# Kernel optimization log

Hardware: AMD Instinct MI355X
Metric: run time of the kernel (lower is better)

## Reference

```python
import jax, jax.numpy as jnp
import numpy as np

N = 50000      # num_nodes
R = 32         # num_relations
H = 16         # hidden channels
C = 16         # num_classes
E = 1600000    # num_edges (avg degree 32)


def setup_inputs() -> dict:
    key = jax.random.key(0)
    ks = jax.random.split(key, 8)
    edge_index = jax.random.randint(ks[0], (2, E), 0, N)
    edge_type = jnp.sort(jax.random.randint(ks[1], (E,), 0, R))
    # per-relation [start, end) slices into the sorted edge list (is_sorted=True)
    starts = jnp.searchsorted(edge_type, jnp.arange(R))
    ends = jnp.searchsorted(edge_type, jnp.arange(R) + 1)
    tensor_slice = jnp.stack([starts, ends], axis=1)
    s = 0.05
    W1 = jax.random.normal(ks[2], (R, N, H), dtype=jnp.float32) * s   # layer-1 per-relation embedding (x=None)
    root1 = jax.random.normal(ks[3], (N, H), dtype=jnp.float32) * s  # root weight acts as embedding when x=None
    bias1 = jax.random.normal(ks[4], (H,), dtype=jnp.float32) * s
    W2 = jax.random.normal(ks[5], (R, H, C), dtype=jnp.float32) * s
    root2 = jax.random.normal(ks[6], (H, C), dtype=jnp.float32) * s
    bias2 = jax.random.normal(ks[7], (C,), dtype=jnp.float32) * s
    return {"edge_index": edge_index, "edge_type": edge_type, "tensor_slice": tensor_slice,
            "W1": W1, "root1": root1, "bias1": bias1,
            "W2": W2, "root2": root2, "bias2": bias2}


def reference(edge_index, edge_type, tensor_slice, W1, root1, bias1, W2, root2, bias2):
    src, dst = edge_index[0], edge_index[1]
    # ---- layer 1: x=None, so per-relation transform is an embedding lookup W1[r][src]
    msg1 = W1[edge_type, src]                                        # [E, H] relation-indexed gather
    h1 = root1 + jax.ops.segment_sum(msg1, dst, num_segments=N) + bias1
    h1 = jax.nn.relu(h1)
    # ---- layer 2: transform all nodes per relation once, then gather per edge
    t = jnp.einsum('nh,rhc->rnc', h1, W2)                            # [R, N, C]
    msg2 = t[edge_type, src]                                         # [E, C]
    h2 = h1 @ root2 + jax.ops.segment_sum(msg2, dst, num_segments=N) + bias2
    return jax.nn.log_softmax(h2, axis=1)
```

## Files before the change

### kernel.cpp

```cpp
#include <hip/hip_runtime.h>
#include <hip/hip_bf16.h>

static constexpr int H = 16;
static constexpr int C = 16;

typedef __attribute__((ext_vector_type(8))) short bf16x8;
typedef __attribute__((ext_vector_type(4))) float f32x4;

static __device__ inline unsigned short f2bf(float x) {
    __hip_bfloat16 b = __float2bfloat16(x);
    return *reinterpret_cast<unsigned short*>(&b);
}
static __device__ inline float bflo(unsigned u) { return __uint_as_float(u << 16); }
static __device__ inline float bfhi(unsigned u) { return __uint_as_float(u & 0xffff0000u); }
static __device__ inline void pk_atomic_bf16(unsigned short* addr, unsigned pk) {
    asm volatile("global_atomic_pk_add_bf16 %0, %1, off" :: "v"(addr), "v"(pk) : "memory");
}

__global__ void k1_scatter(const int* __restrict__ srcv, const int* __restrict__ dstv,
                           const int* __restrict__ etv, const float* __restrict__ W1,
                           unsigned short* __restrict__ acc1, int E, int N) {
    int t = blockIdx.x * blockDim.x + threadIdx.x;
    int g = t >> 3;
    int cp = t & 7;
    int e0 = g << 2;
    if (e0 >= E) return;
    int n = min(4, E - e0);
    int s[4], d[4], r[4];
#pragma unroll
    for (int i = 0; i < 4; ++i) {
        int e = e0 + ((i < n) ? i : 0);
        s[i] = srcv[e]; d[i] = dstv[e]; r[i] = etv[e];
    }
    float2 v[4];
#pragma unroll
    for (int i = 0; i < 4; ++i)
        v[i] = *(const float2*)(W1 + ((size_t)r[i] * N + (size_t)s[i]) * H + (cp << 1));
#pragma unroll
    for (int i = 0; i < 4; ++i)
        if (i < n) {
            unsigned pk = ((unsigned)f2bf(v[i].y) << 16) | f2bf(v[i].x);
            pk_atomic_bf16(acc1 + ((size_t)d[i] << 4) + (cp << 1), pk);
        }
}

__global__ void k2_fin1(const float* __restrict__ root1, const float* __restrict__ bias1,
                        const unsigned short* __restrict__ acc1, float* __restrict__ h1,
                        unsigned int* __restrict__ h1bf, int total4) {
    int i = blockIdx.x * blockDim.x + threadIdx.x;
    if (i >= total4) return;
    float4 rv = ((const float4*)root1)[i];
    uint2 av = ((const uint2*)acc1)[i];
    float4 bv = ((const float4*)bias1)[i & 3];
    float4 o;
    o.x = fmaxf(rv.x + bflo(av.x) + bv.x, 0.0f);
    o.y = fmaxf(rv.y + bfhi(av.x) + bv.y, 0.0f);
    o.z = fmaxf(rv.z + bflo(av.y) + bv.z, 0.0f);
    o.w = fmaxf(rv.w + bfhi(av.y) + bv.w, 0.0f);
    ((float4*)h1)[i] = o;
    uint2 p;
    p.x = ((unsigned)f2bf(o.y) << 16) | f2bf(o.x);
    p.y = ((unsigned)f2bf(o.w) << 16) | f2bf(o.z);
    ((uint2*)h1bf)[i] = p;
}

__global__ void k0_prep(const int* __restrict__ ts, int* __restrict__ chunk_off, int R) {
    if (blockIdx.x == 0 && threadIdx.x == 0) {
        int acc = 0;
        for (int r = 0; r < R; ++r) {
            chunk_off[r] = acc;
            int cnt = ts[2 * r + 1] - ts[2 * r];
            acc += (cnt + 15) >> 4;
        }
        chunk_off[R] = acc;
    }
}

__global__ void k0_cast(const float* __restrict__ W2, unsigned short* __restrict__ w2t,
                        int total ) {
    int i = blockIdx.x * blockDim.x + threadIdx.x;
    if (i >= total) return;
    int r = i >> 8;
    int kc = i & 255;
    int k = kc >> 4;
    int c = kc & 15;
    w2t[(r << 8) + (c << 4) + k] = f2bf(W2[i]);
}

__global__ void k3_mfma(const int* __restrict__ srcv, const int* __restrict__ dstv,
                        const int* __restrict__ ts, const int* __restrict__ chunk_off,
                        const unsigned short* __restrict__ h1bf,
                        const unsigned short* __restrict__ w2t,
                        unsigned short* __restrict__ acc2, int R) {
    int w = (blockIdx.x * blockDim.x + threadIdx.x) >> 6;
    int l = threadIdx.x & 63;
    int total = chunk_off[R];
    if (w >= total) return;
    int lo = 0, hi = R;
    while (hi - lo > 1) {
        int mid = (lo + hi) >> 1;
        if (chunk_off[mid] <= w) lo = mid; else hi = mid;
    }
    int r = lo;
    int e0 = ts[2 * r] + ((w - chunk_off[r]) << 4);
    int eend = ts[2 * r + 1];
    int n_e = min(16, eend - e0);

    int rowA = l & 15;
    int kg = l >> 4;
    int eA = e0 + min(rowA, n_e - 1);
    int s = srcv[eA];

    bf16x8 a = {0, 0, 0, 0, 0, 0, 0, 0};
    bf16x8 b = {0, 0, 0, 0, 0, 0, 0, 0};
    if (kg < 2) {
        a = *(const bf16x8*)(h1bf + ((size_t)s << 4) + (kg << 3));
        b = *(const bf16x8*)(w2t + ((size_t)r << 8) + (rowA << 4) + (kg << 3));
    }
    f32x4 d = {0.f, 0.f, 0.f, 0.f};
    d = __builtin_amdgcn_mfma_f32_16x16x32_bf16(a, b, d, 0, 0, 0);

    int c = l & 15;
#pragma unroll
    for (int j = 0; j < 4; ++j) {
        float o = __shfl_xor(d[j], 1);
        int row = (kg << 2) + j;
        if (((l & 1) == 0) && row < n_e) {
            int dd = dstv[e0 + row];
            unsigned pk = ((unsigned)f2bf(o) << 16) | f2bf(d[j]);
            pk_atomic_bf16(acc2 + ((size_t)dd << 4) + c, pk);
        }
    }
}

__global__ void k4_fin2(const float* __restrict__ h1, const unsigned short* __restrict__ acc2,
                        const float* __restrict__ root2, const float* __restrict__ bias2,
                        float* __restrict__ out, int N) {
    int n = blockIdx.x * blockDim.x + threadIdx.x;
    if (n >= N) return;
    const float* hr = h1 + (size_t)n * H;
    float h[16];
#pragma unroll
    for (int k = 0; k < 16; ++k) h[k] = hr[k];
    const uint4* ap = (const uint4*)(acc2 + (size_t)n * 16);
    uint4 a0 = ap[0], a1 = ap[1];
    float av[16] = {bflo(a0.x), bfhi(a0.x), bflo(a0.y), bfhi(a0.y),
                    bflo(a0.z), bfhi(a0.z), bflo(a0.w), bfhi(a0.w),
                    bflo(a1.x), bfhi(a1.x), bflo(a1.y), bfhi(a1.y),
                    bflo(a1.z), bfhi(a1.z), bflo(a1.w), bfhi(a1.w)};
    float* o = out + (size_t)n * C;
    float z[16];
#pragma unroll
    for (int c = 0; c < 16; ++c) {
        float acc = av[c] + bias2[c];
#pragma unroll
        for (int k = 0; k < 16; ++k) acc += h[k] * root2[k * C + c];
        z[c] = acc;
    }
    float m = z[0];
#pragma unroll
    for (int c = 1; c < 16; ++c) m = fmaxf(m, z[c]);
    float se = 0.f;
#pragma unroll
    for (int c = 0; c < 16; ++c) se += __expf(z[c] - m);
    float lse = m + __logf(se);
#pragma unroll
    for (int c = 0; c < 16; ++c) o[c] = z[c] - lse;
}

extern "C" void kernel_launch(void* const* d_in, const int* in_sizes, int n_in,
                              void* d_out, int out_size, void* d_ws, size_t ws_size,
                              hipStream_t stream) {
    const int*   edge_index   = (const int*)d_in[0];
    const int*   edge_type    = (const int*)d_in[1];
    const int*   tensor_slice = (const int*)d_in[2];
    const float* W1    = (const float*)d_in[3];
    const float* root1 = (const float*)d_in[4];
    const float* bias1 = (const float*)d_in[5];
    const float* W2    = (const float*)d_in[6];
    const float* root2 = (const float*)d_in[7];
    const float* bias2 = (const float*)d_in[8];
    float* out = (float*)d_out;

    const int E = in_sizes[0] / 2;
    const int N = in_sizes[4] / H;
    const int R = in_sizes[2] / 2;
    const int* srcv = edge_index;
    const int* dstv = edge_index + E;

    char* p = (char*)d_ws;
    unsigned short* acc1 = (unsigned short*)p;   p += (size_t)N * 16 * 2;
    float* h1 = (float*)p;                       p += (size_t)N * 16 * 4;
    unsigned short* h1bf = (unsigned short*)p;   p += (size_t)N * 16 * 2;
    unsigned short* w2t = (unsigned short*)p;    p += (size_t)R * 256 * 2;
    unsigned short* acc2 = (unsigned short*)p;   p += (size_t)N * 16 * 2;
    int* chunk_off = (int*)p;

    hipMemsetAsync(acc1, 0, (size_t)N * 16 * 2, stream);
    hipMemsetAsync(acc2, 0, (size_t)N * 16 * 2, stream);

    const int B = 256;
    k0_prep<<<1, 64, 0, stream>>>(tensor_slice, chunk_off, R);
    k0_cast<<<(R * 256 + B - 1) / B, B, 0, stream>>>(W2, w2t, R * 256);
    long long g1 = ((long long)E + 3) / 4;
    long long t1 = g1 * 8;
    k1_scatter<<<(int)((t1 + B - 1) / B), B, 0, stream>>>(srcv, dstv, edge_type, W1, acc1, E, N);
    int total4 = N * H / 4;
    k2_fin1<<<(total4 + B - 1) / B, B, 0, stream>>>(root1, bias1, acc1, h1,
                                                    (unsigned int*)h1bf, total4);
    long long waves_ub = (long long)((E + 15) / 16) + R;
    long long thr = waves_ub * 64;
    k3_mfma<<<(int)((thr + B - 1) / B), B, 0, stream>>>(srcv, dstv, tensor_slice, chunk_off,
                                                        h1bf, w2t, acc2, R);
    k4_fin2<<<(N + B - 1) / B, B, 0, stream>>>(h1, acc2, root2, bias2, out, N);
}
```

Baseline: 197.1 us.

## Batch four MFMA chunks per wave, precompute chunk map, drop fp32 h1

The layer-2 kernel now handles four 16-edge chunks per wave, using a precomputed chunk-to-(edge start, relation, count) map in place of a per-wave binary search. Destination indices are loaded once per row and shared across the wave with shuffles. Layer-1 scatter threads now each process eight edges instead of four, which raises memory-level parallelism. The fp32 h1 buffer is removed and the final kernel reads bf16 h1, cutting write and read traffic at a small precision cost in the root2 term. An extra small kernel launch is added to build the chunk map.

```diff
diff --git a/kernel.cpp b/kernel.cpp
--- a/kernel.cpp
+++ b/kernel.cpp
@@ -23,21 +23,21 @@
     int t = blockIdx.x * blockDim.x + threadIdx.x;
     int g = t >> 3;
     int cp = t & 7;
-    int e0 = g << 2;
+    int e0 = g << 3;
     if (e0 >= E) return;
-    int n = min(4, E - e0);
-    int s[4], d[4], r[4];
-#pragma unroll
-    for (int i = 0; i < 4; ++i) {
+    int n = min(8, E - e0);
+    int s[8], d[8], r[8];
+#pragma unroll
+    for (int i = 0; i < 8; ++i) {
         int e = e0 + ((i < n) ? i : 0);
         s[i] = srcv[e]; d[i] = dstv[e]; r[i] = etv[e];
     }
-    float2 v[4];
-#pragma unroll
-    for (int i = 0; i < 4; ++i)
+    float2 v[8];
+#pragma unroll
+    for (int i = 0; i < 8; ++i)
         v[i] = *(const float2*)(W1 + ((size_t)r[i] * N + (size_t)s[i]) * H + (cp << 1));
 #pragma unroll
-    for (int i = 0; i < 4; ++i)
+    for (int i = 0; i < 8; ++i)
         if (i < n) {
             unsigned pk = ((unsigned)f2bf(v[i].y) << 16) | f2bf(v[i].x);
             pk_atomic_bf16(acc1 + ((size_t)d[i] << 4) + (cp << 1), pk);
@@ -45,7 +45,7 @@
 }
 
 __global__ void k2_fin1(const float* __restrict__ root1, const float* __restrict__ bias1,
-                        const unsigned short* __restrict__ acc1, float* __restrict__ h1,
+                        const unsigned short* __restrict__ acc1,
                         unsigned int* __restrict__ h1bf, int total4) {
     int i = blockIdx.x * blockDim.x + threadIdx.x;
     if (i >= total4) return;
@@ -57,7 +57,6 @@
     o.y = fmaxf(rv.y + bfhi(av.x) + bv.y, 0.0f);
     o.z = fmaxf(rv.z + bflo(av.y) + bv.z, 0.0f);
     o.w = fmaxf(rv.w + bfhi(av.y) + bv.w, 0.0f);
-    ((float4*)h1)[i] = o;
     uint2 p;
     p.x = ((unsigned)f2bf(o.y) << 16) | f2bf(o.x);
     p.y = ((unsigned)f2bf(o.w) << 16) | f2bf(o.z);
@@ -74,6 +73,25 @@
         }
         chunk_off[R] = acc;
     }
+}
+
+__global__ void k0_chunkmap(const int* __restrict__ ts, const int* __restrict__ chunk_off,
+                            int* __restrict__ cmap_e0, int* __restrict__ cmap_rn,
+                            int R, int UB) {
+    int c = blockIdx.x * blockDim.x + threadIdx.x;
+    if (c >= UB) return;
+    int T = chunk_off[R];
+    if (c >= T) return;
+    int lo = 0, hi = R;
+    while (hi - lo > 1) {
+        int mid = (lo + hi) >> 1;
+        if (chunk_off[mid] <= c) lo = mid; else hi = mid;
+    }
+    int r = lo;
+    int e0 = ts[2 * r] + ((c - chunk_off[r]) << 4);
+    int n = min(16, ts[2 * r + 1] - e0);
+    cmap_e0[c] = e0;
+    cmap_rn[c] = (n << 8) | r;
 }
 
 __global__ void k0_cast(const float* __restrict__ W2, unsigned short* __restrict__ w2t,
@@ -88,60 +106,81 @@
 }
 
 __global__ void k3_mfma(const int* __restrict__ srcv, const int* __restrict__ dstv,
-                        const int* __restrict__ ts, const int* __restrict__ chunk_off,
+                        const int* __restrict__ cmap_e0, const int* __restrict__ cmap_rn,
+                        const int* __restrict__ chunk_off,
                         const unsigned short* __restrict__ h1bf,
                         const unsigned short* __restrict__ w2t,
                         unsigned short* __restrict__ acc2, int R) {
     int w = (blockIdx.x * blockDim.x + threadIdx.x) >> 6;
     int l = threadIdx.x & 63;
-    int total = chunk_off[R];
-    if (w >= total) return;
-    int lo = 0, hi = R;
-    while (hi - lo > 1) {
-        int mid = (lo + hi) >> 1;
-        if (chunk_off[mid] <= w) lo = mid; else hi = mid;
-    }
-    int r = lo;
-    int e0 = ts[2 * r] + ((w - chunk_off[r]) << 4);
-    int eend = ts[2 * r + 1];
-    int n_e = min(16, eend - e0);
+    int T = chunk_off[R];
+    int c0 = w << 2;
+    if (c0 >= T) return;
 
     int rowA = l & 15;
     int kg = l >> 4;
-    int eA = e0 + min(rowA, n_e - 1);
-    int s = srcv[eA];
-
-    bf16x8 a = {0, 0, 0, 0, 0, 0, 0, 0};
-    bf16x8 b = {0, 0, 0, 0, 0, 0, 0, 0};
-    if (kg < 2) {
-        a = *(const bf16x8*)(h1bf + ((size_t)s << 4) + (kg << 3));
-        b = *(const bf16x8*)(w2t + ((size_t)r << 8) + (rowA << 4) + (kg << 3));
-    }
-    f32x4 d = {0.f, 0.f, 0.f, 0.f};
-    d = __builtin_amdgcn_mfma_f32_16x16x32_bf16(a, b, d, 0, 0, 0);
-
+
+    int e0[4], rr[4], nn[4], s[4], dd[4];
+#pragma unroll
+    for (int q = 0; q < 4; ++q) {
+        int cq = c0 + q;
+        bool ok = cq < T;
+        int e = ok ? cmap_e0[cq] : 0;
+        int rn = ok ? cmap_rn[cq] : 0;
+        e0[q] = e;
+        rr[q] = rn & 255;
+        nn[q] = rn >> 8;
+    }
+#pragma unroll
+    for (int q = 0; q < 4; ++q) {
+        int eA = e0[q] + max(0, min(rowA, nn[q] - 1));
+        s[q] = srcv[eA];
+        dd[q] = dstv[eA];
+    }
+    bf16x8 a[4], b[4];
+#pragma unroll
+    for (int q = 0; q < 4; ++q) {
+        bf16x8 z = {0, 0, 0, 0, 0, 0, 0, 0};
+        a[q] = z; b[q] = z;
+        if (kg < 2) {
+            a[q] = *(const bf16x8*)(h1bf + ((size_t)s[q] << 4) + (kg << 3));
+            b[q] = *(const bf16x8*)(w2t + ((size_t)rr[q] << 8) + (rowA << 4) + (kg << 3));
+        }
+    }
+    f32x4 d[4];
+#pragma unroll
+    for (int q = 0; q < 4; ++q) {
+        f32x4 z4 = {0.f, 0.f, 0.f, 0.f};
+        d[q] = __builtin_amdgcn_mfma_f32_16x16x32_bf16(a[q], b[q], z4, 0, 0, 0);
+    }
     int c = l & 15;
 #pragma unroll
-    for (int j = 0; j < 4; ++j) {
-        float o = __shfl_xor(d[j], 1);
-        int row = (kg << 2) + j;
-        if (((l & 1) == 0) && row < n_e) {
-            int dd = dstv[e0 + row];
-            unsigned pk = ((unsigned)f2bf(o) << 16) | f2bf(d[j]);
-            pk_atomic_bf16(acc2 + ((size_t)dd << 4) + c, pk);
-        }
-    }
-}
-
-__global__ void k4_fin2(const float* __restrict__ h1, const unsigned short* __restrict__ acc2,
+    for (int q = 0; q < 4; ++q) {
+#pragma unroll
+        for (int j = 0; j < 4; ++j) {
+            int row = (kg << 2) + j;
+            float o = __shfl_xor(d[q][j], 1);
+            int ddv = __shfl(dd[q], row);
+            if (((l & 1) == 0) && row < nn[q]) {
+                unsigned pk = ((unsigned)f2bf(o) << 16) | f2bf(d[q][j]);
+                pk_atomic_bf16(acc2 + ((size_t)ddv << 4) + c, pk);
+            }
+        }
+    }
+}
+
+__global__ void k4_fin2(const unsigned short* __restrict__ h1bf,
+                        const unsigned short* __restrict__ acc2,
                         const float* __restrict__ root2, const float* __restrict__ bias2,
                         float* __restrict__ out, int N) {
     int n = blockIdx.x * blockDim.x + threadIdx.x;
     if (n >= N) return;
-    const float* hr = h1 + (size_t)n * H;
-    float h[16];
-#pragma unroll
-    for (int k = 0; k < 16; ++k) h[k] = hr[k];
+    const uint4* hp = (const uint4*)(h1bf + (size_t)n * 16);
+    uint4 h0 = hp[0], h1 = hp[1];
+    float h[16] = {bflo(h0.x), bfhi(h0.x), bflo(h0.y), bfhi(h0.y),
+                   bflo(h0.z), bfhi(h0.z), bflo(h0.w), bfhi(h0.w),
+                   bflo(h1.x), bfhi(h1.x), bflo(h1.y), bfhi(h1.y),
+                   bflo(h1.z), bfhi(h1.z), bflo(h1.w), bfhi(h1.w)};
     const uint4* ap = (const uint4*)(acc2 + (size_t)n * 16);
     uint4 a0 = ap[0], a1 = ap[1];
     float av[16] = {bflo(a0.x), bfhi(a0.x), bflo(a0.y), bfhi(a0.y),
@@ -188,29 +227,34 @@
     const int* srcv = edge_index;
     const int* dstv = edge_index + E;
 
+    const int UB = (E + 15) / 16 + R;
     char* p = (char*)d_ws;
     unsigned short* acc1 = (unsigned short*)p;   p += (size_t)N * 16 * 2;
-    float* h1 = (float*)p;                       p += (size_t)N * 16 * 4;
     unsigned short* h1bf = (unsigned short*)p;   p += (size_t)N * 16 * 2;
     unsigned short* w2t = (unsigned short*)p;    p += (size_t)R * 256 * 2;
     unsigned short* acc2 = (unsigned short*)p;   p += (size_t)N * 16 * 2;
-    int* chunk_off = (int*)p;
+    int* chunk_off = (int*)p;                    p += (size_t)(R + 1) * 4;
+    p = (char*)(((uintptr_t)p + 15) & ~(uintptr_t)15);
+    int* cmap_e0 = (int*)p;                      p += (size_t)UB * 4;
+    int* cmap_rn = (int*)p;
 
     hipMemsetAsync(acc1, 0, (size_t)N * 16 * 2, stream);
     hipMemsetAsync(acc2, 0, (size_t)N * 16 * 2, stream);
 
     const int B = 256;
     k0_prep<<<1, 64, 0, stream>>>(tensor_slice, chunk_off, R);
+    k0_chunkmap<<<(UB + B - 1) / B, B, 0, stream>>>(tensor_slice, chunk_off,
+                                                    cmap_e0, cmap_rn, R, UB);
     k0_cast<<<(R * 256 + B - 1) / B, B, 0, stream>>>(W2, w2t, R * 256);
-    long long g1 = ((long long)E + 3) / 4;
+    long long g1 = ((long long)E + 7) / 8;
     long long t1 = g1 * 8;
     k1_scatter<<<(int)((t1 + B - 1) / B), B, 0, stream>>>(srcv, dstv, edge_type, W1, acc1, E, N);
     int total4 = N * H / 4;
-    k2_fin1<<<(total4 + B - 1) / B, B, 0, stream>>>(root1, bias1, acc1, h1,
+    k2_fin1<<<(total4 + B - 1) / B, B, 0, stream>>>(root1, bias1, acc1,
                                                     (unsigned int*)h1bf, total4);
-    long long waves_ub = (long long)((E + 15) / 16) + R;
-    long long thr = waves_ub * 64;
-    k3_mfma<<<(int)((thr + B - 1) / B), B, 0, stream>>>(srcv, dstv, tensor_slice, chunk_off,
-                                                        h1bf, w2t, acc2, R);
-    k4_fin2<<<(N + B - 1) / B, B, 0, stream>>>(h1, acc2, root2, bias2, out, N);
-}
+    long long waves = ((long long)UB + 3) / 4;
+    long long thr = waves * 64;
+    k3_mfma<<<(int)((thr + B - 1) / B), B, 0, stream>>>(srcv, dstv, cmap_e0, cmap_rn,
+                                                        chunk_off, h1bf, w2t, acc2, R);
+    k4_fin2<<<(N + B - 1) / B, B, 0, stream>>>(h1bf, acc2, root2, bias2, out, N);
+}
```

After: 192.6 us. 2.3% less time.
